# Performance work log

Measured on AMD Instinct MI355X. Metric: run time of the kernel, lower is better.

## Reference

```python
import jax, jax.numpy as jnp
import numpy as np

EPS = 1e-5
NEG_SLOPE = 0.01  # torch leaky_relu default

def _bn_relu(x, g, b):
    # BatchNorm2d with 1 channel in training mode: normalize over all elems
    m = x.mean()
    v = ((x - m) ** 2).mean()  # biased variance, as torch uses for normalization
    return jax.nn.relu((x - m) / jnp.sqrt(v + EPS) * g + b)

def setup_inputs() -> dict:
    key = jax.random.key(0)
    ks = jax.random.split(key, 8)
    N, K, IN, D = 65536, 32, 128, 64
    return {
        "h": jax.random.normal(ks[0], (N, IN), jnp.float32),
        "W_fc": jax.random.normal(ks[1], (D, IN), jnp.float32) * (1.0 / np.sqrt(IN)),
        "a_attn": jax.random.normal(ks[2], (2 * D,), jnp.float32) * (1.0 / np.sqrt(2 * D)),
        "w_row": jax.random.normal(ks[3], (2, D), jnp.float32) * (1.0 / np.sqrt(2 * D)),
        "b_row": jnp.zeros((1,), jnp.float32),
        "w_col": jax.random.normal(ks[4], (K, D), jnp.float32) * (1.0 / np.sqrt(K)),
        "b_col": jnp.zeros((1,), jnp.float32),
        "g_row": jnp.ones((1,), jnp.float32),
        "beta_row": jnp.zeros((1,), jnp.float32),
        "g_col": jnp.ones((1,), jnp.float32),
        "beta_col": jnp.zeros((1,), jnp.float32),
        "src_idx": jax.random.randint(ks[5], (N * K,), 0, N, jnp.int32),
    }

def reference(h, W_fc, a_attn, w_row, b_row, w_col, b_col,
              g_row, beta_row, g_col, beta_col, src_idx):
    N = h.shape[0]
    D = W_fc.shape[0]
    K = w_col.shape[0]
    z = h @ W_fc.T                                   # [N, D]
    # attention logits; cat([zs, zd]) @ a == zs @ a[:D] + zd @ a[D:] (no bias)
    e_src = z @ a_attn[:D]                           # [N]
    e_dst = z @ a_attn[D:]                           # [N]
    e = e_src[src_idx].reshape(N, K) + e_dst[:, None]  # [N, K] (dst = repeat(arange(N), K))
    e = jax.nn.leaky_relu(e, NEG_SLOPE)
    alpha = jax.nn.softmax(e, axis=1)                # segment softmax over neighbors
    zs = z[src_idx].reshape(N, K, D)                 # mailbox gather
    feats = alpha[..., None] * zs                    # [N, K, D]
    # convrow: Conv2d kernel (2, D) over [N,1,K,D] -> [N, K-1]
    row = (jnp.einsum('nkd,d->nk', feats[:, :-1], w_row[0])
           + jnp.einsum('nkd,d->nk', feats[:, 1:], w_row[1]) + b_row)
    row = _bn_relu(row, g_row, beta_row)
    # convcol: Conv2d kernel (K, 1) -> [N, D]
    col = jnp.einsum('nkd,kd->nd', feats, w_col) + b_col
    col = _bn_relu(col, g_col, beta_col)
    return jnp.concatenate([row, col], axis=1)       # [N, K-1+D]
```

## Files before the change

### kernel.cpp

```cpp
#include <hip/hip_runtime.h>
#include <hip/hip_bf16.h>

#define KK 32
#define INF 128
#define DD 64
#define OW 95

typedef __attribute__((ext_vector_type(8))) short s8v;
typedef __attribute__((ext_vector_type(4))) float f32x4;

__device__ __forceinline__ float bf2f(unsigned short u) {
    union { unsigned int i; float f; } cv; cv.i = (unsigned int)u << 16; return cv.f;
}
__device__ __forceinline__ unsigned short f2bf(float f) {
    __hip_bfloat16 h = __float2bfloat16(f);
    return *reinterpret_cast<unsigned short*>(&h);
}
__device__ __forceinline__ s8v pack8(float4 a, float4 b) {
    union { unsigned short u[8]; s8v v; } r;
    r.u[0] = f2bf(a.x); r.u[1] = f2bf(a.y); r.u[2] = f2bf(a.z); r.u[3] = f2bf(a.w);
    r.u[4] = f2bf(b.x); r.u[5] = f2bf(b.y); r.u[6] = f2bf(b.z); r.u[7] = f2bf(b.w);
    return r.v;
}

__global__ __launch_bounds__(256) void k_gemm(
    const float* __restrict__ h, const float* __restrict__ Wfc,
    const float* __restrict__ a_attn, const float* __restrict__ w_row,
    __hip_bfloat16* __restrict__ zb, float* __restrict__ aux)
{
    __shared__ __align__(16) unsigned short zs[64][72];
    __shared__ float vec[4][68];

    int t = threadIdx.x, lane = t & 63, wave = t >> 6;
    int g = lane >> 4, c = lane & 15;
    size_t rowbase = (size_t)blockIdx.x * 64;

    {
        int i = t & 63, ty = t >> 6;
        vec[ty][i] = (ty == 0) ? a_attn[i]
                   : (ty == 1) ? w_row[i]
                   : (ty == 2) ? w_row[64 + i]
                               : a_attn[64 + i];
    }

    const float* hrow = h + (rowbase + (size_t)wave * 16 + c) * INF;
    s8v afr[4];
#pragma unroll
    for (int kt = 0; kt < 4; ++kt) {
        const float* p = hrow + kt * 32 + g * 8;
        afr[kt] = pack8(*(const float4*)p, *(const float4*)(p + 4));
    }
    s8v bfr[4][4];
#pragma unroll
    for (int nt = 0; nt < 4; ++nt) {
        const float* wrow = Wfc + (size_t)(nt * 16 + c) * INF;
#pragma unroll
        for (int kt = 0; kt < 4; ++kt) {
            const float* p = wrow + kt * 32 + g * 8;
            bfr[nt][kt] = pack8(*(const float4*)p, *(const float4*)(p + 4));
        }
    }

    f32x4 acc[4];
#pragma unroll
    for (int nt = 0; nt < 4; ++nt) {
        acc[nt] = (f32x4){0.f, 0.f, 0.f, 0.f};
#pragma unroll
        for (int kt = 0; kt < 4; ++kt)
            acc[nt] = __builtin_amdgcn_mfma_f32_16x16x32_bf16(afr[kt], bfr[nt][kt], acc[nt], 0, 0, 0);
    }

#pragma unroll
    for (int nt = 0; nt < 4; ++nt)
#pragma unroll
        for (int r = 0; r < 4; ++r)
            zs[wave * 16 + g * 4 + r][nt * 16 + c] = f2bf(acc[nt][r]);
    __syncthreads();

#pragma unroll
    for (int it = 0; it < 2; ++it) {
        int f = t + it * 256;
        int row = f >> 3, ch = f & 7;
        uint4 v = *(const uint4*)((const char*)&zs[row][0] + ch * 16);
        *(uint4*)((char*)zb + (rowbase + row) * 128 + ch * 16) = v;
    }

    {
        int row = t >> 2, ty = t & 3;
        const uint4* zr = (const uint4*)&zs[row][0];
        float s = 0.f;
#pragma unroll
        for (int q = 0; q < 8; ++q) {
            uint4 v = zr[q];
            const float* vp = &vec[ty][q * 8];
            s = fmaf(bf2f((unsigned short)(v.x & 0xffff)), vp[0], s);
            s = fmaf(bf2f((unsigned short)(v.x >> 16)),    vp[1], s);
            s = fmaf(bf2f((unsigned short)(v.y & 0xffff)), vp[2], s);
            s = fmaf(bf2f((unsigned short)(v.y >> 16)),    vp[3], s);
            s = fmaf(bf2f((unsigned short)(v.z & 0xffff)), vp[4], s);
            s = fmaf(bf2f((unsigned short)(v.z >> 16)),    vp[5], s);
            s = fmaf(bf2f((unsigned short)(v.w & 0xffff)), vp[6], s);
            s = fmaf(bf2f((unsigned short)(v.w >> 16)),    vp[7], s);
        }
        aux[rowbase * 4 + t] = s;
    }
}

__global__ __launch_bounds__(256) void k_gat(
    const unsigned short* __restrict__ zb, const float4* __restrict__ aux,
    const int* __restrict__ src_idx, const float* __restrict__ w_col,
    const float* __restrict__ b_row, const float* __restrict__ b_col,
    float* __restrict__ out, float4* __restrict__ partials)
{
    __shared__ uint2  s_as[4][2][32];
    __shared__ float  s_wc[2048];
    __shared__ float4 s_part[8];

    int t = threadIdx.x, lane = t & 63, wave = t >> 6;
    int half = lane >> 5, hk = lane & 31;
    int n = blockIdx.x * 8 + wave * 2 + half;

#pragma unroll
    for (int i = 0; i < 8; ++i) s_wc[t + 256 * i] = w_col[t + 256 * i];

    const float* auxf = (const float*)aux;
    int sk = src_idx[(size_t)n * KK + hk];
    float4 ax = aux[sk];
    float ed = auxf[n * 4 + 3];
    float e = ax.x + ed;
    e = e > 0.f ? e : 0.01f * e;
    float m = e;
#pragma unroll
    for (int s = 16; s; s >>= 1) m = fmaxf(m, __shfl_xor(m, s));
    float p = __expf(e - m);
    float sum = p;
#pragma unroll
    for (int s = 16; s; s >>= 1) sum += __shfl_xor(sum, s);
    float alpha = p / sum;
    s_as[wave][half][hk] = make_uint2(__float_as_uint(alpha), (unsigned int)sk * 128u);
    float t1 = alpha * ax.z;
    float tn = __shfl_down(t1, 1);
    float rowv = fmaf(alpha, ax.y, tn) + b_row[0];
    float rs = 0.f, rss = 0.f;
    if (hk < 31) {
        out[(size_t)n * OW + hk] = rowv;
        rs = rowv; rss = rowv * rowv;
    }
    __syncthreads();

    const char* zbase = (const char*)zb;
    const unsigned int* pas = (const unsigned int*)&s_as[wave][half][0];
    unsigned int dof = (unsigned int)hk * 4u;

    unsigned int zv[32];
#pragma unroll
    for (int kk = 0; kk < 32; ++kk) {
        unsigned int so = pas[kk * 2 + 1];
        zv[kk] = *(const unsigned int*)(zbase + (size_t)(so + dof));
    }

    float acc0 = 0.f, acc1 = 0.f;
#pragma unroll
    for (int kk = 0; kk < 32; ++kk) {
        float al = __uint_as_float(pas[kk * 2]);
        float2 wcp = *(const float2*)&s_wc[kk * 64 + hk * 2];
        union { unsigned int u; float f; } lo, hi;
        lo.u = zv[kk] << 16;
        hi.u = zv[kk] & 0xffff0000u;
        acc0 = fmaf(al * wcp.x, lo.f, acc0);
        acc1 = fmaf(al * wcp.y, hi.f, acc1);
    }
    float bc = b_col[0];
    float colv0 = acc0 + bc, colv1 = acc1 + bc;
    out[(size_t)n * OW + 31 + 2 * hk] = colv0;
    out[(size_t)n * OW + 32 + 2 * hk] = colv1;

    float cs = colv0 + colv1, css = colv0 * colv0 + colv1 * colv1;
#pragma unroll
    for (int s = 16; s; s >>= 1) {
        rs  += __shfl_xor(rs, s);
        rss += __shfl_xor(rss, s);
        cs  += __shfl_xor(cs, s);
        css += __shfl_xor(css, s);
    }
    if (hk == 0) s_part[wave * 2 + half] = make_float4(rs, rss, cs, css);
    __syncthreads();
    if (t == 0) {
        float4 a = make_float4(0.f, 0.f, 0.f, 0.f);
#pragma unroll
        for (int i = 0; i < 8; ++i) {
            a.x += s_part[i].x; a.y += s_part[i].y;
            a.z += s_part[i].z; a.w += s_part[i].w;
        }
        partials[blockIdx.x] = a;
    }
}

__global__ __launch_bounds__(256) void k_stats(
    const float4* __restrict__ partials, int nb,
    const float* __restrict__ g_row, const float* __restrict__ beta_row,
    const float* __restrict__ g_col, const float* __restrict__ beta_col,
    float* __restrict__ bnp, int N)
{
    __shared__ float4 sp[256];
    int t = threadIdx.x;
    float4 acc = make_float4(0.f, 0.f, 0.f, 0.f);
    for (int i = t; i < nb; i += 256) {
        float4 p = partials[i];
        acc.x += p.x; acc.y += p.y; acc.z += p.z; acc.w += p.w;
    }
    sp[t] = acc;
    __syncthreads();
    for (int s = 128; s > 0; s >>= 1) {
        if (t < s) {
            sp[t].x += sp[t + s].x; sp[t].y += sp[t + s].y;
            sp[t].z += sp[t + s].z; sp[t].w += sp[t + s].w;
        }
        __syncthreads();
    }
    if (t == 0) {
        float nrow = (float)N * 31.0f;
        float ncol = (float)N * 64.0f;
        float mr = sp[0].x / nrow;
        float vr = sp[0].y / nrow - mr * mr;
        float sr = g_row[0] / sqrtf(vr + 1e-5f);
        float br = beta_row[0] - mr * sr;
        float mc = sp[0].z / ncol;
        float vc = sp[0].w / ncol - mc * mc;
        float sc = g_col[0] / sqrtf(vc + 1e-5f);
        float bc = beta_col[0] - mc * sc;
        bnp[0] = sr; bnp[1] = br; bnp[2] = sc; bnp[3] = bc;
    }
}

__global__ __launch_bounds__(256) void k_apply(
    float* __restrict__ out, const float* __restrict__ bnp, int total4)
{
    float sr = bnp[0], br = bnp[1], sc = bnp[2], bc = bnp[3];
    int idx = blockIdx.x * 256 + threadIdx.x;
    int stride = gridDim.x * 256;
    for (; idx < total4; idx += stride) {
        int i = idx * 4;
        float4 x = *(float4*)(out + i);
        int c = i % OW;
        float r[4] = {x.x, x.y, x.z, x.w};
#pragma unroll
        for (int j = 0; j < 4; ++j) {
            int cj = c + j; if (cj >= OW) cj -= OW;
            float y = (cj < 31) ? fmaf(r[j], sr, br) : fmaf(r[j], sc, bc);
            r[j] = fmaxf(y, 0.0f);
        }
        *(float4*)(out + i) = make_float4(r[0], r[1], r[2], r[3]);
    }
}

extern "C" void kernel_launch(void* const* d_in, const int* in_sizes, int n_in,
                              void* d_out, int out_size, void* d_ws, size_t ws_size,
                              hipStream_t stream) {
    const float* h        = (const float*)d_in[0];
    const float* Wfc      = (const float*)d_in[1];
    const float* a_attn   = (const float*)d_in[2];
    const float* w_row    = (const float*)d_in[3];
    const float* b_row    = (const float*)d_in[4];
    const float* w_col    = (const float*)d_in[5];
    const float* b_col    = (const float*)d_in[6];
    const float* g_row    = (const float*)d_in[7];
    const float* beta_row = (const float*)d_in[8];
    const float* g_col    = (const float*)d_in[9];
    const float* beta_col = (const float*)d_in[10];
    const int*   src_idx  = (const int*)d_in[11];

    int N = in_sizes[0] / INF;
    float* out = (float*)d_out;

    __hip_bfloat16* zb = (__hip_bfloat16*)d_ws;
    float4* aux      = (float4*)((char*)d_ws + (size_t)N * DD * 2);
    float4* partials = aux + N;
    float*  bnp      = (float*)(partials + N / 8);

    k_gemm <<<N / 64, 256, 0, stream>>>(h, Wfc, a_attn, w_row, zb, (float*)aux);
    k_gat  <<<N / 8,  256, 0, stream>>>((const unsigned short*)zb, aux, src_idx,
                                        w_col, b_row, b_col, out, partials);
    k_stats<<<1,      256, 0, stream>>>(partials, N / 8, g_row, beta_row, g_col, beta_col, bnp, N);
    int total4 = (N * OW) / 4;
    k_apply<<<2048,   256, 0, stream>>>(out, bnp, total4);
}
```

Baseline: 175.5 us.

## Vectorize z gathers to 16-byte loads and issue them before softmax

The mailbox gather of bf16 z rows now uses uint4 (16-byte) loads, with each lane covering 8 dims of 8 of the 32 neighbors, instead of 32 separate 4-byte loads per lane. The loads are issued before the softmax using a shared source-offset array, so gather latency overlaps the attention computation. Partial column sums are then reduced across lane groups with shuffles. Launch bounds are raised to request 4 blocks per CU. The cost is extra shuffle reductions and a dynamically indexed acc array, which may spill to scratch.

```diff
diff --git a/kernel.cpp b/kernel.cpp
--- a/kernel.cpp
+++ b/kernel.cpp
@@ -106,25 +106,39 @@
     }
 }
 
-__global__ __launch_bounds__(256) void k_gat(
+__global__ __launch_bounds__(256, 4) void k_gat(
     const unsigned short* __restrict__ zb, const float4* __restrict__ aux,
     const int* __restrict__ src_idx, const float* __restrict__ w_col,
     const float* __restrict__ b_row, const float* __restrict__ b_col,
     float* __restrict__ out, float4* __restrict__ partials)
 {
-    __shared__ uint2  s_as[4][2][32];
-    __shared__ float  s_wc[2048];
-    __shared__ float4 s_part[8];
+    __shared__ float        s_wc[2048];
+    __shared__ unsigned int s_al[4][2][32];
+    __shared__ unsigned int s_soff[4][2][32];
+    __shared__ float4       s_part[8];
 
     int t = threadIdx.x, lane = t & 63, wave = t >> 6;
-    int half = lane >> 5, hk = lane & 31;
+    int half = lane >> 5, hl = lane & 31;
     int n = blockIdx.x * 8 + wave * 2 + half;
 
+    int sk = src_idx[(size_t)n * KK + hl];
+    s_soff[wave][half][hl] = (unsigned int)sk * 128u;
+
 #pragma unroll
     for (int i = 0; i < 8; ++i) s_wc[t + 256 * i] = w_col[t + 256 * i];
 
+    const char* zbase = (const char*)zb;
+    unsigned int doff = (unsigned int)(hl & 7) * 16u;
+    int rsel = hl >> 3;
+    const unsigned int* soffp = &s_soff[wave][half][0];
+    uint4 zv[8];
+#pragma unroll
+    for (int i = 0; i < 8; ++i) {
+        unsigned int so = soffp[4 * i + rsel];
+        zv[i] = *(const uint4*)(zbase + (size_t)(so + doff));
+    }
+
     const float* auxf = (const float*)aux;
-    int sk = src_idx[(size_t)n * KK + hk];
     float4 ax = aux[sk];
     float ed = auxf[n * 4 + 3];
     float e = ax.x + ed;
@@ -137,43 +151,52 @@
 #pragma unroll
     for (int s = 16; s; s >>= 1) sum += __shfl_xor(sum, s);
     float alpha = p / sum;
-    s_as[wave][half][hk] = make_uint2(__float_as_uint(alpha), (unsigned int)sk * 128u);
+    s_al[wave][half][hl] = __float_as_uint(alpha);
     float t1 = alpha * ax.z;
     float tn = __shfl_down(t1, 1);
     float rowv = fmaf(alpha, ax.y, tn) + b_row[0];
     float rs = 0.f, rss = 0.f;
-    if (hk < 31) {
-        out[(size_t)n * OW + hk] = rowv;
+    if (hl < 31) {
+        out[(size_t)n * OW + hl] = rowv;
         rs = rowv; rss = rowv * rowv;
     }
     __syncthreads();
 
-    const char* zbase = (const char*)zb;
-    const unsigned int* pas = (const unsigned int*)&s_as[wave][half][0];
-    unsigned int dof = (unsigned int)hk * 4u;
-
-    unsigned int zv[32];
-#pragma unroll
-    for (int kk = 0; kk < 32; ++kk) {
-        unsigned int so = pas[kk * 2 + 1];
-        zv[kk] = *(const unsigned int*)(zbase + (size_t)(so + dof));
-    }
-
-    float acc0 = 0.f, acc1 = 0.f;
-#pragma unroll
-    for (int kk = 0; kk < 32; ++kk) {
-        float al = __uint_as_float(pas[kk * 2]);
-        float2 wcp = *(const float2*)&s_wc[kk * 64 + hk * 2];
+    float acc[8] = {0.f, 0.f, 0.f, 0.f, 0.f, 0.f, 0.f, 0.f};
+    const unsigned int* alp = &s_al[wave][half][0];
+#pragma unroll
+    for (int i = 0; i < 8; ++i) {
+        int r = 4 * i + rsel;
+        float al = __uint_as_float(alp[r]);
+        const float* wcp = &s_wc[r * 64 + (hl & 7) * 8];
+        float4 w0 = *(const float4*)wcp;
+        float4 w1 = *(const float4*)(wcp + 4);
+        uint4 v = zv[i];
         union { unsigned int u; float f; } lo, hi;
-        lo.u = zv[kk] << 16;
-        hi.u = zv[kk] & 0xffff0000u;
-        acc0 = fmaf(al * wcp.x, lo.f, acc0);
-        acc1 = fmaf(al * wcp.y, hi.f, acc1);
+        lo.u = v.x << 16; hi.u = v.x & 0xffff0000u;
+        acc[0] = fmaf(al * w0.x, lo.f, acc[0]);
+        acc[1] = fmaf(al * w0.y, hi.f, acc[1]);
+        lo.u = v.y << 16; hi.u = v.y & 0xffff0000u;
+        acc[2] = fmaf(al * w0.z, lo.f, acc[2]);
+        acc[3] = fmaf(al * w0.w, hi.f, acc[3]);
+        lo.u = v.z << 16; hi.u = v.z & 0xffff0000u;
+        acc[4] = fmaf(al * w1.x, lo.f, acc[4]);
+        acc[5] = fmaf(al * w1.y, hi.f, acc[5]);
+        lo.u = v.w << 16; hi.u = v.w & 0xffff0000u;
+        acc[6] = fmaf(al * w1.z, lo.f, acc[6]);
+        acc[7] = fmaf(al * w1.w, hi.f, acc[7]);
+    }
+#pragma unroll
+    for (int j = 0; j < 8; ++j) {
+        acc[j] += __shfl_xor(acc[j], 8);
+        acc[j] += __shfl_xor(acc[j], 16);
     }
     float bc = b_col[0];
-    float colv0 = acc0 + bc, colv1 = acc1 + bc;
-    out[(size_t)n * OW + 31 + 2 * hk] = colv0;
-    out[(size_t)n * OW + 32 + 2 * hk] = colv1;
+    float colv0 = acc[rsel * 2]     + bc;
+    float colv1 = acc[rsel * 2 + 1] + bc;
+    int d0 = (hl & 7) * 8 + rsel * 2;
+    out[(size_t)n * OW + 31 + d0]     = colv0;
+    out[(size_t)n * OW + 31 + d0 + 1] = colv1;
 
     float cs = colv0 + colv1, css = colv0 * colv0 + colv1 * colv1;
 #pragma unroll
@@ -183,7 +206,7 @@
         cs  += __shfl_xor(cs, s);
         css += __shfl_xor(css, s);
     }
-    if (hk == 0) s_part[wave * 2 + half] = make_float4(rs, rss, cs, css);
+    if (hl == 0) s_part[wave * 2 + half] = make_float4(rs, rss, cs, css);
     __syncthreads();
     if (t == 0) {
         float4 a = make_float4(0.f, 0.f, 0.f, 0.f);
```

Result: slower. 184.8 us (+5.3%).

## Split neighbor gather into two address-range passes and fuse BN stats via atomics

Applied to the files above, without the earlier changes.

The GAT gather loop now runs two passes. Each pass reads only rows from one half of the bf16 z table; neighbors that fall in the other half get a zero weight. The goal is to keep each pass's working set within a per-XCD L2-sized region, at the cost of issuing twice as many gather loads. The separate stats reduction kernel is removed: blocks now atomically add their partial sums into a global buffer that is cleared by a memset and seeded with the gamma/beta values by a tiny prep kernel, and the apply kernel computes the BN scale and shift itself. Output stores become nontemporal, and the GEMM builds its weight fragments inside the MFMA loop instead of preloading them all.

```diff
diff --git a/kernel.cpp b/kernel.cpp
--- a/kernel.cpp
+++ b/kernel.cpp
@@ -13,8 +13,8 @@
     union { unsigned int i; float f; } cv; cv.i = (unsigned int)u << 16; return cv.f;
 }
 __device__ __forceinline__ unsigned short f2bf(float f) {
-    __hip_bfloat16 h = __float2bfloat16(f);
-    return *reinterpret_cast<unsigned short*>(&h);
+    __hip_bfloat16 hh = __float2bfloat16(f);
+    return *reinterpret_cast<unsigned short*>(&hh);
 }
 __device__ __forceinline__ s8v pack8(float4 a, float4 b) {
     union { unsigned short u[8]; s8v v; } r;
@@ -50,24 +50,17 @@
         const float* p = hrow + kt * 32 + g * 8;
         afr[kt] = pack8(*(const float4*)p, *(const float4*)(p + 4));
     }
-    s8v bfr[4][4];
+    f32x4 acc[4];
 #pragma unroll
     for (int nt = 0; nt < 4; ++nt) {
+        acc[nt] = (f32x4){0.f, 0.f, 0.f, 0.f};
         const float* wrow = Wfc + (size_t)(nt * 16 + c) * INF;
 #pragma unroll
         for (int kt = 0; kt < 4; ++kt) {
             const float* p = wrow + kt * 32 + g * 8;
-            bfr[nt][kt] = pack8(*(const float4*)p, *(const float4*)(p + 4));
-        }
-    }
-
-    f32x4 acc[4];
-#pragma unroll
-    for (int nt = 0; nt < 4; ++nt) {
-        acc[nt] = (f32x4){0.f, 0.f, 0.f, 0.f};
-#pragma unroll
-        for (int kt = 0; kt < 4; ++kt)
-            acc[nt] = __builtin_amdgcn_mfma_f32_16x16x32_bf16(afr[kt], bfr[nt][kt], acc[nt], 0, 0, 0);
+            s8v bfr = pack8(*(const float4*)p, *(const float4*)(p + 4));
+            acc[nt] = __builtin_amdgcn_mfma_f32_16x16x32_bf16(afr[kt], bfr, acc[nt], 0, 0, 0);
+        }
     }
 
 #pragma unroll
@@ -110,21 +103,21 @@
     const unsigned short* __restrict__ zb, const float4* __restrict__ aux,
     const int* __restrict__ src_idx, const float* __restrict__ w_col,
     const float* __restrict__ b_row, const float* __restrict__ b_col,
-    float* __restrict__ out, float4* __restrict__ partials)
+    float* __restrict__ out, float* __restrict__ sums)
 {
     __shared__ uint2  s_as[4][2][32];
     __shared__ float  s_wc[2048];
-    __shared__ float4 s_part[8];
+    __shared__ float4 s_part[4];
 
     int t = threadIdx.x, lane = t & 63, wave = t >> 6;
-    int half = lane >> 5, hk = lane & 31;
+    int half = lane >> 5, hl = lane & 31;
     int n = blockIdx.x * 8 + wave * 2 + half;
 
 #pragma unroll
     for (int i = 0; i < 8; ++i) s_wc[t + 256 * i] = w_col[t + 256 * i];
 
     const float* auxf = (const float*)aux;
-    int sk = src_idx[(size_t)n * KK + hk];
+    int sk = src_idx[(size_t)n * KK + hl];
     float4 ax = aux[sk];
     float ed = auxf[n * 4 + 3];
     float e = ax.x + ed;
@@ -137,106 +130,74 @@
 #pragma unroll
     for (int s = 16; s; s >>= 1) sum += __shfl_xor(sum, s);
     float alpha = p / sum;
-    s_as[wave][half][hk] = make_uint2(__float_as_uint(alpha), (unsigned int)sk * 128u);
+    s_as[wave][half][hl] = make_uint2(__float_as_uint(alpha), (unsigned int)sk * 128u);
     float t1 = alpha * ax.z;
     float tn = __shfl_down(t1, 1);
     float rowv = fmaf(alpha, ax.y, tn) + b_row[0];
     float rs = 0.f, rss = 0.f;
-    if (hk < 31) {
-        out[(size_t)n * OW + hk] = rowv;
+    if (hl < 31) {
+        __builtin_nontemporal_store(rowv, &out[(size_t)n * OW + hl]);
         rs = rowv; rss = rowv * rowv;
     }
     __syncthreads();
 
     const char* zbase = (const char*)zb;
-    const unsigned int* pas = (const unsigned int*)&s_as[wave][half][0];
-    unsigned int dof = (unsigned int)hk * 4u;
-
-    unsigned int zv[32];
-#pragma unroll
-    for (int kk = 0; kk < 32; ++kk) {
-        unsigned int so = pas[kk * 2 + 1];
-        zv[kk] = *(const unsigned int*)(zbase + (size_t)(so + dof));
-    }
+    const uint2* pas = &s_as[wave][half][0];
+    unsigned int dof = (unsigned int)hl * 4u;
 
     float acc0 = 0.f, acc1 = 0.f;
 #pragma unroll
-    for (int kk = 0; kk < 32; ++kk) {
-        float al = __uint_as_float(pas[kk * 2]);
-        float2 wcp = *(const float2*)&s_wc[kk * 64 + hk * 2];
-        union { unsigned int u; float f; } lo, hi;
-        lo.u = zv[kk] << 16;
-        hi.u = zv[kk] & 0xffff0000u;
-        acc0 = fmaf(al * wcp.x, lo.f, acc0);
-        acc1 = fmaf(al * wcp.y, hi.f, acc1);
+    for (int pass = 0; pass < 2; ++pass) {
+        unsigned int base = pass ? 4194304u : 0u;
+#pragma unroll
+        for (int kk = 0; kk < 32; ++kk) {
+            uint2 av = pas[kk];
+            unsigned int so = (av.y & 0x3FFFFFu) + base;
+            float al = ((av.y >> 22) == (unsigned)pass) ? __uint_as_float(av.x) : 0.f;
+            unsigned int zv = *(const unsigned int*)(zbase + (size_t)(so + dof));
+            float2 wcp = *(const float2*)&s_wc[kk * 64 + hl * 2];
+            union { unsigned int u; float f; } lo, hi;
+            lo.u = zv << 16;
+            hi.u = zv & 0xffff0000u;
+            acc0 = fmaf(al * wcp.x, lo.f, acc0);
+            acc1 = fmaf(al * wcp.y, hi.f, acc1);
+        }
     }
     float bc = b_col[0];
     float colv0 = acc0 + bc, colv1 = acc1 + bc;
-    out[(size_t)n * OW + 31 + 2 * hk] = colv0;
-    out[(size_t)n * OW + 32 + 2 * hk] = colv1;
+    __builtin_nontemporal_store(colv0, &out[(size_t)n * OW + 31 + 2 * hl]);
+    __builtin_nontemporal_store(colv1, &out[(size_t)n * OW + 32 + 2 * hl]);
 
     float cs = colv0 + colv1, css = colv0 * colv0 + colv1 * colv1;
 #pragma unroll
-    for (int s = 16; s; s >>= 1) {
+    for (int s = 32; s; s >>= 1) {
         rs  += __shfl_xor(rs, s);
         rss += __shfl_xor(rss, s);
         cs  += __shfl_xor(cs, s);
         css += __shfl_xor(css, s);
     }
-    if (hk == 0) s_part[wave * 2 + half] = make_float4(rs, rss, cs, css);
+    if (lane == 0) s_part[wave] = make_float4(rs, rss, cs, css);
     __syncthreads();
     if (t == 0) {
-        float4 a = make_float4(0.f, 0.f, 0.f, 0.f);
-#pragma unroll
-        for (int i = 0; i < 8; ++i) {
-            a.x += s_part[i].x; a.y += s_part[i].y;
-            a.z += s_part[i].z; a.w += s_part[i].w;
-        }
-        partials[blockIdx.x] = a;
-    }
-}
-
-__global__ __launch_bounds__(256) void k_stats(
-    const float4* __restrict__ partials, int nb,
-    const float* __restrict__ g_row, const float* __restrict__ beta_row,
-    const float* __restrict__ g_col, const float* __restrict__ beta_col,
-    float* __restrict__ bnp, int N)
-{
-    __shared__ float4 sp[256];
-    int t = threadIdx.x;
-    float4 acc = make_float4(0.f, 0.f, 0.f, 0.f);
-    for (int i = t; i < nb; i += 256) {
-        float4 p = partials[i];
-        acc.x += p.x; acc.y += p.y; acc.z += p.z; acc.w += p.w;
-    }
-    sp[t] = acc;
-    __syncthreads();
-    for (int s = 128; s > 0; s >>= 1) {
-        if (t < s) {
-            sp[t].x += sp[t + s].x; sp[t].y += sp[t + s].y;
-            sp[t].z += sp[t + s].z; sp[t].w += sp[t + s].w;
-        }
-        __syncthreads();
-    }
-    if (t == 0) {
-        float nrow = (float)N * 31.0f;
-        float ncol = (float)N * 64.0f;
-        float mr = sp[0].x / nrow;
-        float vr = sp[0].y / nrow - mr * mr;
-        float sr = g_row[0] / sqrtf(vr + 1e-5f);
-        float br = beta_row[0] - mr * sr;
-        float mc = sp[0].z / ncol;
-        float vc = sp[0].w / ncol - mc * mc;
-        float sc = g_col[0] / sqrtf(vc + 1e-5f);
-        float bc = beta_col[0] - mc * sc;
-        bnp[0] = sr; bnp[1] = br; bnp[2] = sc; bnp[3] = bc;
+        float4 p0 = s_part[0], p1 = s_part[1], p2 = s_part[2], p3 = s_part[3];
+        atomicAdd(&sums[0], p0.x + p1.x + p2.x + p3.x);
+        atomicAdd(&sums[1], p0.y + p1.y + p2.y + p3.y);
+        atomicAdd(&sums[2], p0.z + p1.z + p2.z + p3.z);
+        atomicAdd(&sums[3], p0.w + p1.w + p2.w + p3.w);
     }
 }
 
 __global__ __launch_bounds__(256) void k_apply(
-    float* __restrict__ out, const float* __restrict__ bnp, int total4)
-{
-    float sr = bnp[0], br = bnp[1], sc = bnp[2], bc = bnp[3];
+    float* __restrict__ out, const float* __restrict__ sums, int N, int total4)
+{
+    float nrow = (float)N * 31.0f, ncol = (float)N * 64.0f;
+    float mr = sums[0] / nrow, vr = sums[1] / nrow - mr * mr;
+    float mc = sums[2] / ncol, vc = sums[3] / ncol - mc * mc;
+    float sr = sums[4] * __frsqrt_rn(vr + 1e-5f);
+    float br = sums[5] - mr * sr;
+    float sc = sums[6] * __frsqrt_rn(vc + 1e-5f);
+    float bc = sums[7] - mc * sc;
+
     int idx = blockIdx.x * 256 + threadIdx.x;
     int stride = gridDim.x * 256;
     for (; idx < total4; idx += stride) {
@@ -251,6 +212,18 @@
             r[j] = fmaxf(y, 0.0f);
         }
         *(float4*)(out + i) = make_float4(r[0], r[1], r[2], r[3]);
+    }
+}
+
+__global__ void k_prep(const float* g_row, const float* beta_row,
+                       const float* g_col, const float* beta_col,
+                       float* sums)
+{
+    if (threadIdx.x == 0) {
+        sums[4] = g_row[0];
+        sums[5] = beta_row[0];
+        sums[6] = g_col[0];
+        sums[7] = beta_col[0];
     }
 }
 
@@ -274,14 +247,14 @@
     float* out = (float*)d_out;
 
     __hip_bfloat16* zb = (__hip_bfloat16*)d_ws;
-    float4* aux      = (float4*)((char*)d_ws + (size_t)N * DD * 2);
-    float4* partials = aux + N;
-    float*  bnp      = (float*)(partials + N / 8);
-
-    k_gemm <<<N / 64, 256, 0, stream>>>(h, Wfc, a_attn, w_row, zb, (float*)aux);
-    k_gat  <<<N / 8,  256, 0, stream>>>((const unsigned short*)zb, aux, src_idx,
-                                        w_col, b_row, b_col, out, partials);
-    k_stats<<<1,      256, 0, stream>>>(partials, N / 8, g_row, beta_row, g_col, beta_col, bnp, N);
+    float* aux  = (float*)((char*)d_ws + (size_t)N * DD * 2);
+    float* sums = aux + (size_t)N * 4;
+
+    hipMemsetAsync(sums, 0, 4 * sizeof(float), stream);
+    k_prep <<<1, 64, 0, stream>>>(g_row, beta_row, g_col, beta_col, sums);
+    k_gemm <<<N / 64, 256, 0, stream>>>(h, Wfc, a_attn, w_row, zb, aux);
+    k_gat  <<<N / 8,  256, 0, stream>>>((const unsigned short*)zb, (const float4*)aux,
+                                        src_idx, w_col, b_row, b_col, out, sums);
     int total4 = (N * OW) / 4;
-    k_apply<<<2048,   256, 0, stream>>>(out, bnp, total4);
-}
+    k_apply<<<2048,   256, 0, stream>>>(out, sums, N, total4);
+}
```

Result: slower. 557.8 us (+217.9%).
